# Optimization experiments

Hardware: AMD Instinct MI355X
Metric: run time of the kernel (lower is better)

## Reference

```python
import jax, jax.numpy as jnp
import numpy as np

C = 256          # channels
K = 7            # kernel_size
GC = 16          # group_channels
G = C // GC      # groups = 16
RED = C // 4     # reduction channels = 64
EPS = 1e-5


def unfold_same(x, k):
    """torch nn.Unfold(k, stride=1, padding=(k-1)//2) -> (b, c, k*k, h, w),
    channel-major patch ordering matching torch (c, kh, kw)."""
    pad = (k - 1) // 2
    xp = jnp.pad(x, ((0, 0), (0, 0), (pad, pad), (pad, pad)))
    h, w = x.shape[2], x.shape[3]
    # fixed k*k=49 slices, vectorized over all data dims
    pats = jnp.stack([xp[:, :, i:i + h, j:j + w]
                      for i in range(k) for j in range(k)], axis=2)
    return pats  # (b, c, k*k, h, w)


def setup_inputs() -> dict:
    key = jax.random.key(0)
    ks = jax.random.split(key, 8)
    b, h, w = 2, 64, 64
    feature_map = jax.random.normal(ks[0], (b, C, h, w), jnp.float32)
    guide_map = jax.random.normal(ks[1], (b, C, h, w), jnp.float32)
    # convs1: 1x1 conv (no bias, followed by BN) + BN params + ReLU
    w1 = jax.random.normal(ks[2], (RED, C), jnp.float32) * (1.0 / np.sqrt(C))
    bn_gamma = jnp.ones((RED,), jnp.float32)
    bn_beta = jnp.zeros((RED,), jnp.float32)
    bn_mean = jax.random.normal(ks[3], (RED,), jnp.float32) * 0.1
    bn_var = jax.random.uniform(ks[4], (RED,), jnp.float32, 0.5, 1.5)
    # convs2: 1x1 conv with bias, out = K^2 * G channels
    w2 = jax.random.normal(ks[5], (K * K * G, RED), jnp.float32) * (1.0 / np.sqrt(RED))
    b2 = jax.random.normal(ks[6], (K * K * G,), jnp.float32) * 0.01
    return dict(feature_map=feature_map, guide_map=guide_map,
                w1=w1, bn_gamma=bn_gamma, bn_beta=bn_beta,
                bn_mean=bn_mean, bn_var=bn_var, w2=w2, b2=b2)


def reference(feature_map, guide_map, w1, bn_gamma, bn_beta, bn_mean, bn_var, w2, b2):
    b, _, h, w = feature_map.shape
    # kernel-generation branch: 1x1 conv -> BN (inference) -> ReLU -> 1x1 conv
    t = jnp.einsum('oc,bchw->bohw', w1, guide_map)
    scale = bn_gamma / jnp.sqrt(bn_var + EPS)
    shift = bn_beta - bn_mean * scale
    t = jax.nn.relu(t * scale[None, :, None, None] + shift[None, :, None, None])
    weight = jnp.einsum('or,brhw->bohw', w2, t) + b2[None, :, None, None]
    weight = weight.reshape(b, G, K * K, h, w)
    # involution: unfold, broadcast per-pixel kernels over group channels, reduce K^2
    pats = unfold_same(feature_map, K).reshape(b, G, GC, K * K, h, w)
    out = jnp.einsum('bgkhw,bgckhw->bgchw', weight, pats).reshape(b, C, h, w)
    return out + feature_map
```

## Files before the change

kernel.cpp:

```cpp
#include <hip/hip_runtime.h>

#define CC  256
#define HW  4096
#define HH  64
#define WW  64
#define RED 64
#define K2  49
#define NG  16
#define GCH 16

typedef __attribute__((ext_vector_type(8))) short bf16x8;
typedef __attribute__((ext_vector_type(4))) float f32x4;

__device__ inline unsigned short f2bf(float f) {
    union { float f; unsigned u; } v; v.f = f;
    unsigned r = v.u + 0x7FFF + ((v.u >> 16) & 1);
    return (unsigned short)(r >> 16);
}

#define TT_ELTS   524288
#define W2BF_ROWS 832

__global__ __launch_bounds__(64) void k1_kernel(
    const float* __restrict__ guide,
    const float* __restrict__ w1,
    const float* __restrict__ gamma,
    const float* __restrict__ beta,
    const float* __restrict__ mean,
    const float* __restrict__ var,
    const float* __restrict__ w2,
    unsigned short* __restrict__ tt,
    unsigned short* __restrict__ w2bf)
{
    const int bid = blockIdx.x;
    const int tid = threadIdx.x;

    if (bid >= 512) {
        const int idx = (bid - 512) * 64 + tid;
        if (idx < (W2BF_ROWS * RED) / 8) {
            unsigned short r8[8];
            if (idx * 8 < K2 * NG * RED) {
                const float4 a = *reinterpret_cast<const float4*>(w2 + idx * 8);
                const float4 b = *reinterpret_cast<const float4*>(w2 + idx * 8 + 4);
                r8[0] = f2bf(a.x); r8[1] = f2bf(a.y); r8[2] = f2bf(a.z); r8[3] = f2bf(a.w);
                r8[4] = f2bf(b.x); r8[5] = f2bf(b.y); r8[6] = f2bf(b.z); r8[7] = f2bf(b.w);
            } else {
                #pragma unroll
                for (int i = 0; i < 8; ++i) r8[i] = 0;
            }
            *reinterpret_cast<uint4*>(w2bf + idx * 8) = *reinterpret_cast<const uint4*>(r8);
        }
        return;
    }

    const int bb = bid >> 8;
    const int y  = (bid >> 2) & 63;
    const int nt = bid & 3;
    const int lm = tid & 15;
    const int lg = tid >> 4;
    const int px = nt * 16 + lm;

    const float* gcol = guide + (size_t)bb * CC * HW + (size_t)y * WW + px;

    f32x4 acc[4] = {f32x4{0,0,0,0}, f32x4{0,0,0,0}, f32x4{0,0,0,0}, f32x4{0,0,0,0}};

    #pragma unroll
    for (int ks = 0; ks < 8; ++ks) {
        const int cbase = ks * 32 + lg * 8;
        union { unsigned short u[8]; bf16x8 v; } B;
        #pragma unroll
        for (int j = 0; j < 8; ++j)
            B.u[j] = f2bf(gcol[(size_t)(cbase + j) * HW]);
        #pragma unroll
        for (int mt = 0; mt < 4; ++mt) {
            const float* ar = w1 + (size_t)(mt * 16 + lm) * CC + cbase;
            const float4 a0 = *reinterpret_cast<const float4*>(ar);
            const float4 a1 = *reinterpret_cast<const float4*>(ar + 4);
            union { unsigned short u[8]; bf16x8 v; } A;
            A.u[0] = f2bf(a0.x); A.u[1] = f2bf(a0.y);
            A.u[2] = f2bf(a0.z); A.u[3] = f2bf(a0.w);
            A.u[4] = f2bf(a1.x); A.u[5] = f2bf(a1.y);
            A.u[6] = f2bf(a1.z); A.u[7] = f2bf(a1.w);
            acc[mt] = __builtin_amdgcn_mfma_f32_16x16x32_bf16(A.v, B.v, acc[mt], 0, 0, 0);
        }
    }

    const size_t ttrow = ((size_t)bb * HW + (size_t)y * WW + px) * RED;
    #pragma unroll
    for (int mt = 0; mt < 4; ++mt) {
        union { unsigned short u[4]; uint2 v; } R;
        #pragma unroll
        for (int rr = 0; rr < 4; ++rr) {
            const int o = mt * 16 + lg * 4 + rr;
            const float sc = gamma[o] * rsqrtf(var[o] + 1e-5f);
            const float sh = beta[o] - mean[o] * sc;
            float v = fmaf(acc[mt][rr], sc, sh);
            v = v > 0.f ? v : 0.f;
            R.u[rr] = f2bf(v);
        }
        *reinterpret_cast<uint2*>(tt + ttrow + mt * 16 + lg * 4) = R.v;
    }
}

__global__ __launch_bounds__(256, 3) void k2_inv_kernel(
    const float* __restrict__ feat,
    const unsigned short* __restrict__ tt,
    const unsigned short* __restrict__ w2bf,
    const float* __restrict__ b2,
    float* __restrict__ out)
{
    __shared__ float wg[2][K2][WW];

    const int bid = blockIdx.x;
    const int bb  = bid >> 9;
    const int y   = (bid >> 3) & 63;
    const int gp  = bid & 7;
    const int tid  = threadIdx.x;
    const int lane = tid & 63;
    const int wv   = __builtin_amdgcn_readfirstlane(tid >> 6);
    const int lm = lane & 15;
    const int lg = lane >> 4;

    {
        const int gi    = wv >> 1;
        const int g     = gp * 2 + gi;
        const int obase = g * K2;
        f32x4 acc[2][4];
        #pragma unroll
        for (int h = 0; h < 2; ++h)
            #pragma unroll
            for (int mt = 0; mt < 4; ++mt) acc[h][mt] = f32x4{0, 0, 0, 0};

        #pragma unroll
        for (int h = 0; h < 2; ++h) {
            const int nt = (wv & 1) * 2 + h;
            const size_t ttb = ((size_t)bb * HW + (size_t)y * WW + nt * 16 + lm) * RED + lg * 8;
            #pragma unroll
            for (int ks = 0; ks < 2; ++ks) {
                const bf16x8 bfr = *reinterpret_cast<const bf16x8*>(tt + ttb + ks * 32);
                #pragma unroll
                for (int mt = 0; mt < 4; ++mt) {
                    const bf16x8 afr = *reinterpret_cast<const bf16x8*>(
                        w2bf + (size_t)(obase + mt * 16 + lm) * RED + ks * 32 + lg * 8);
                    acc[h][mt] = __builtin_amdgcn_mfma_f32_16x16x32_bf16(afr, bfr, acc[h][mt], 0, 0, 0);
                }
            }
        }
        #pragma unroll
        for (int h = 0; h < 2; ++h)
            #pragma unroll
            for (int mt = 0; mt < 4; ++mt)
                #pragma unroll
                for (int rr = 0; rr < 4; ++rr) {
                    const int o2 = mt * 16 + lg * 4 + rr;
                    if (o2 < K2)
                        wg[gi][o2][(wv & 1) * 32 + h * 16 + lm] = acc[h][mt][rr] + b2[obase + o2];
                }
    }
    __syncthreads();

    const int gh = tid >> 7;
    const int cp = (tid >> 4) & 7;
    const int xq = tid & 15;
    const int x0 = xq * 4;
    const int c0 = (gp * 2 + gh) * GCH + cp * 2;
    const float* fb0 = feat + ((size_t)bb * CC + c0) * HW;
    const float* fb1 = fb0 + HW;

    const float4 rr0 = *reinterpret_cast<const float4*>(fb0 + (size_t)y * WW + x0);
    const float4 rr1 = *reinterpret_cast<const float4*>(fb1 + (size_t)y * WW + x0);
    float s00 = rr0.x, s01 = rr0.y, s02 = rr0.z, s03 = rr0.w;
    float s10 = rr1.x, s11 = rr1.y, s12 = rr1.z, s13 = rr1.w;

    #pragma unroll
    for (int i = 0; i < 7; ++i) {
        const int yy = y + i - 3;
        if (yy < 0 || yy >= HH) continue;
        const float* fr0 = fb0 + (size_t)yy * WW;
        const float* fr1 = fb1 + (size_t)yy * WW;

        float4 L0 = make_float4(0.f, 0.f, 0.f, 0.f), L1 = L0;
        float4 R0 = L0, R1 = L0;
        const float4 M0 = *reinterpret_cast<const float4*>(fr0 + x0);
        const float4 M1 = *reinterpret_cast<const float4*>(fr1 + x0);
        if (xq > 0)  { L0 = *reinterpret_cast<const float4*>(fr0 + x0 - 4);
                       L1 = *reinterpret_cast<const float4*>(fr1 + x0 - 4); }
        if (xq < 15) { R0 = *reinterpret_cast<const float4*>(fr0 + x0 + 4);
                       R1 = *reinterpret_cast<const float4*>(fr1 + x0 + 4); }
        const float b0[12] = {L0.x, L0.y, L0.z, L0.w, M0.x, M0.y, M0.z, M0.w,
                              R0.x, R0.y, R0.z, R0.w};
        const float b1[12] = {L1.x, L1.y, L1.z, L1.w, M1.x, M1.y, M1.z, M1.w,
                              R1.x, R1.y, R1.z, R1.w};

        #pragma unroll
        for (int jx = 0; jx < 7; ++jx) {
            const float4 w4 = *reinterpret_cast<const float4*>(&wg[gh][i * 7 + jx][x0]);
            s00 = fmaf(w4.x, b0[jx + 1], s00);
            s01 = fmaf(w4.y, b0[jx + 2], s01);
            s02 = fmaf(w4.z, b0[jx + 3], s02);
            s03 = fmaf(w4.w, b0[jx + 4], s03);
            s10 = fmaf(w4.x, b1[jx + 1], s10);
            s11 = fmaf(w4.y, b1[jx + 2], s11);
            s12 = fmaf(w4.z, b1[jx + 3], s12);
            s13 = fmaf(w4.w, b1[jx + 4], s13);
        }
    }

    float4 o0; o0.x = s00; o0.y = s01; o0.z = s02; o0.w = s03;
    float4 o1; o1.x = s10; o1.y = s11; o1.z = s12; o1.w = s13;
    float* ob = out + ((size_t)bb * CC + c0) * HW + (size_t)y * WW + x0;
    *reinterpret_cast<float4*>(ob)      = o0;
    *reinterpret_cast<float4*>(ob + HW) = o1;
}

__global__ __launch_bounds__(512, 1) void crossinv_fused_kernel(
    const float* __restrict__ feat, const float* __restrict__ guide,
    const float* __restrict__ w1, const float* __restrict__ gamma,
    const float* __restrict__ beta, const float* __restrict__ mean,
    const float* __restrict__ var, const float* __restrict__ w2,
    const float* __restrict__ b2, float* __restrict__ out)
{
    __shared__ float st[RED][WW];
    __shared__ float wg[K2][WW];
    const int bid  = blockIdx.x;
    const int bb   = bid >> 7;
    const int y    = (bid >> 1) & 63;
    const int gsel = bid & 1;
    const int lane = threadIdx.x & 63;
    const int wv   = __builtin_amdgcn_readfirstlane(threadIdx.x >> 6);

    const float* gptr = guide + (size_t)bb * CC * HW + (size_t)y * WW + lane;
    float acc[8];
    #pragma unroll
    for (int j = 0; j < 8; ++j) acc[j] = 0.f;
    for (int c0 = 0; c0 < CC; c0 += 4) {
        const float gv0 = gptr[(c0 + 0) * HW];
        const float gv1 = gptr[(c0 + 1) * HW];
        const float gv2 = gptr[(c0 + 2) * HW];
        const float gv3 = gptr[(c0 + 3) * HW];
        #pragma unroll
        for (int j = 0; j < 8; ++j) {
            const int o = wv + 8 * j;
            const float4 wr = *reinterpret_cast<const float4*>(w1 + o * CC + c0);
            acc[j] = fmaf(wr.x, gv0, acc[j]);
            acc[j] = fmaf(wr.y, gv1, acc[j]);
            acc[j] = fmaf(wr.z, gv2, acc[j]);
            acc[j] = fmaf(wr.w, gv3, acc[j]);
        }
    }
    #pragma unroll
    for (int j = 0; j < 8; ++j) {
        const int o = wv + 8 * j;
        const float sc = gamma[o] * rsqrtf(var[o] + 1e-5f);
        const float sh = beta[o] - mean[o] * sc;
        const float v  = fmaf(acc[j], sc, sh);
        st[o][lane] = v > 0.f ? v : 0.f;
    }
    __syncthreads();
    for (int gi = 0; gi < 8; ++gi) {
        const int gg    = gsel * 8 + gi;
        const int obase = gg * K2;
        float accw[7];
        #pragma unroll
        for (int j = 0; j < 7; ++j) {
            const int o2 = wv + 8 * j;
            accw[j] = (o2 < K2) ? b2[obase + o2] : 0.f;
        }
        for (int r0 = 0; r0 < RED; r0 += 4) {
            const float t0 = st[r0 + 0][lane];
            const float t1 = st[r0 + 1][lane];
            const float t2 = st[r0 + 2][lane];
            const float t3 = st[r0 + 3][lane];
            #pragma unroll
            for (int j = 0; j < 7; ++j) {
                const int o2 = wv + 8 * j;
                if (o2 < K2) {
                    const float4 wr = *reinterpret_cast<const float4*>(
                        w2 + (size_t)(obase + o2) * RED + r0);
                    accw[j] = fmaf(wr.x, t0, accw[j]);
                    accw[j] = fmaf(wr.y, t1, accw[j]);
                    accw[j] = fmaf(wr.z, t2, accw[j]);
                    accw[j] = fmaf(wr.w, t3, accw[j]);
                }
            }
        }
        #pragma unroll
        for (int j = 0; j < 7; ++j) {
            const int o2 = wv + 8 * j;
            if (o2 < K2) wg[o2][lane] = accw[j];
        }
        __syncthreads();
        #pragma unroll
        for (int cc2 = 0; cc2 < 2; ++cc2) {
            const int cc = wv * 2 + cc2;
            const int cch = gg * GCH + cc;
            const float* fb = feat + ((size_t)bb * CC + cch) * HW;
            float sum = fb[y * WW + lane];
            #pragma unroll
            for (int i = 0; i < 7; ++i) {
                const int yy = y + i - 3;
                if (yy < 0 || yy >= HH) continue;
                const float* frow = fb + yy * WW;
                #pragma unroll
                for (int jx = 0; jx < 7; ++jx) {
                    const int xx = lane + jx - 3;
                    const float fv = (xx >= 0 && xx < WW) ? frow[xx] : 0.f;
                    sum = fmaf(wg[i * 7 + jx][lane], fv, sum);
                }
            }
            out[((size_t)bb * CC + cch) * HW + (size_t)y * WW + lane] = sum;
        }
        __syncthreads();
    }
}

extern "C" void kernel_launch(void* const* d_in, const int* in_sizes, int n_in,
                              void* d_out, int out_size, void* d_ws, size_t ws_size,
                              hipStream_t stream) {
    const float* feat  = (const float*)d_in[0];
    const float* guide = (const float*)d_in[1];
    const float* w1    = (const float*)d_in[2];
    const float* gamma = (const float*)d_in[3];
    const float* beta  = (const float*)d_in[4];
    const float* mean  = (const float*)d_in[5];
    const float* var   = (const float*)d_in[6];
    const float* w2    = (const float*)d_in[7];
    const float* b2    = (const float*)d_in[8];
    float* out = (float*)d_out;

    const size_t need = (size_t)TT_ELTS * 2 + (size_t)W2BF_ROWS * RED * 2;
    if (ws_size >= need) {
        unsigned short* tt   = (unsigned short*)d_ws;
        unsigned short* w2bf = tt + TT_ELTS;
        hipLaunchKernelGGL(k1_kernel, dim3(512 + 104), dim3(64), 0, stream,
                           guide, w1, gamma, beta, mean, var, w2, tt, w2bf);
        hipLaunchKernelGGL(k2_inv_kernel, dim3(1024), dim3(256), 0, stream,
                           feat, tt, w2bf, b2, out);
    } else {
        hipLaunchKernelGGL(crossinv_fused_kernel, dim3(256), dim3(512), 0, stream,
                           feat, guide, w1, gamma, beta, mean, var, w2, b2, out);
    }
}
```

Measured before the change: 30.19 us.

## Tile involution over four rows per block and pack k1 into 256-thread blocks

The involution kernel now gives each block one group and four output rows instead of one row and two groups. Each loaded feature row is reused across up to four output rows, so a block reads 10 rows per channel instead of 7 per output row, and each w2bf A-fragment is reused across four column tiles in the MFMA loop. The residual add is folded into the i==3 tap. The first kernel packs four 64-lane work units into each 256-thread block, giving 154 blocks instead of 616. The trade-offs are fewer blocks (512) for the involution stage, a larger shared buffer padded to 68 columns, and more accumulator registers.

```diff
diff --git a/kernel.cpp b/kernel.cpp
--- a/kernel.cpp
+++ b/kernel.cpp
@@ -21,7 +21,7 @@
 #define TT_ELTS   524288
 #define W2BF_ROWS 832
 
-__global__ __launch_bounds__(64) void k1_kernel(
+__global__ __launch_bounds__(256) void k1_kernel(
     const float* __restrict__ guide,
     const float* __restrict__ w1,
     const float* __restrict__ gamma,
@@ -32,11 +32,11 @@
     unsigned short* __restrict__ tt,
     unsigned short* __restrict__ w2bf)
 {
-    const int bid = blockIdx.x;
-    const int tid = threadIdx.x;
-
-    if (bid >= 512) {
-        const int idx = (bid - 512) * 64 + tid;
+    const int lane = threadIdx.x & 63;
+    const int unit = blockIdx.x * 4 + __builtin_amdgcn_readfirstlane(threadIdx.x >> 6);
+
+    if (unit >= 512) {
+        const int idx = (unit - 512) * 64 + lane;
         if (idx < (W2BF_ROWS * RED) / 8) {
             unsigned short r8[8];
             if (idx * 8 < K2 * NG * RED) {
@@ -53,11 +53,11 @@
         return;
     }
 
-    const int bb = bid >> 8;
-    const int y  = (bid >> 2) & 63;
-    const int nt = bid & 3;
-    const int lm = tid & 15;
-    const int lg = tid >> 4;
+    const int bb = unit >> 8;
+    const int y  = (unit >> 2) & 63;
+    const int nt = unit & 3;
+    const int lm = lane & 15;
+    const int lg = lane >> 4;
     const int px = nt * 16 + lm;
 
     const float* gcol = guide + (size_t)bb * CC * HW + (size_t)y * WW + px;
@@ -109,108 +109,116 @@
     const float* __restrict__ b2,
     float* __restrict__ out)
 {
-    __shared__ float wg[2][K2][WW];
+    __shared__ float wg[4][K2][68];
 
     const int bid = blockIdx.x;
-    const int bb  = bid >> 9;
-    const int y   = (bid >> 3) & 63;
-    const int gp  = bid & 7;
+    const int bb  = bid >> 8;
+    const int yt  = (bid >> 4) & 15;
+    const int g   = bid & 15;
+    const int y0  = yt * 4;
     const int tid  = threadIdx.x;
     const int lane = tid & 63;
     const int wv   = __builtin_amdgcn_readfirstlane(tid >> 6);
     const int lm = lane & 15;
     const int lg = lane >> 4;
+    const int obase = g * K2;
 
     {
-        const int gi    = wv >> 1;
-        const int g     = gp * 2 + gi;
-        const int obase = g * K2;
-        f32x4 acc[2][4];
-        #pragma unroll
-        for (int h = 0; h < 2; ++h)
-            #pragma unroll
-            for (int mt = 0; mt < 4; ++mt) acc[h][mt] = f32x4{0, 0, 0, 0};
-
-        #pragma unroll
-        for (int h = 0; h < 2; ++h) {
-            const int nt = (wv & 1) * 2 + h;
-            const size_t ttb = ((size_t)bb * HW + (size_t)y * WW + nt * 16 + lm) * RED + lg * 8;
-            #pragma unroll
-            for (int ks = 0; ks < 2; ++ks) {
-                const bf16x8 bfr = *reinterpret_cast<const bf16x8*>(tt + ttb + ks * 32);
+        const int y = y0 + wv;
+        f32x4 acc[4][4];
+        #pragma unroll
+        for (int nt = 0; nt < 4; ++nt)
+            #pragma unroll
+            for (int mt = 0; mt < 4; ++mt) acc[nt][mt] = f32x4{0, 0, 0, 0};
+
+        #pragma unroll
+        for (int ks = 0; ks < 2; ++ks) {
+            bf16x8 bfr[4];
+            #pragma unroll
+            for (int nt = 0; nt < 4; ++nt)
+                bfr[nt] = *reinterpret_cast<const bf16x8*>(
+                    tt + ((size_t)bb * HW + (size_t)y * WW + nt * 16 + lm) * RED + ks * 32 + lg * 8);
+            #pragma unroll
+            for (int mt = 0; mt < 4; ++mt) {
+                const bf16x8 afr = *reinterpret_cast<const bf16x8*>(
+                    w2bf + (size_t)(obase + mt * 16 + lm) * RED + ks * 32 + lg * 8);
                 #pragma unroll
-                for (int mt = 0; mt < 4; ++mt) {
-                    const bf16x8 afr = *reinterpret_cast<const bf16x8*>(
-                        w2bf + (size_t)(obase + mt * 16 + lm) * RED + ks * 32 + lg * 8);
-                    acc[h][mt] = __builtin_amdgcn_mfma_f32_16x16x32_bf16(afr, bfr, acc[h][mt], 0, 0, 0);
-                }
-            }
-        }
-        #pragma unroll
-        for (int h = 0; h < 2; ++h)
+                for (int nt = 0; nt < 4; ++nt)
+                    acc[nt][mt] = __builtin_amdgcn_mfma_f32_16x16x32_bf16(afr, bfr[nt], acc[nt][mt], 0, 0, 0);
+            }
+        }
+        float bias[4][4];
+        #pragma unroll
+        for (int mt = 0; mt < 4; ++mt)
+            #pragma unroll
+            for (int rr = 0; rr < 4; ++rr) {
+                const int o2 = mt * 16 + lg * 4 + rr;
+                bias[mt][rr] = (o2 < K2) ? b2[obase + o2] : 0.f;
+            }
+        #pragma unroll
+        for (int nt = 0; nt < 4; ++nt)
             #pragma unroll
             for (int mt = 0; mt < 4; ++mt)
                 #pragma unroll
                 for (int rr = 0; rr < 4; ++rr) {
                     const int o2 = mt * 16 + lg * 4 + rr;
                     if (o2 < K2)
-                        wg[gi][o2][(wv & 1) * 32 + h * 16 + lm] = acc[h][mt][rr] + b2[obase + o2];
+                        wg[wv][o2][nt * 16 + lm] = acc[nt][mt][rr] + bias[mt][rr];
                 }
     }
     __syncthreads();
 
-    const int gh = tid >> 7;
-    const int cp = (tid >> 4) & 7;
+    const int cl = tid >> 4;
     const int xq = tid & 15;
     const int x0 = xq * 4;
-    const int c0 = (gp * 2 + gh) * GCH + cp * 2;
-    const float* fb0 = feat + ((size_t)bb * CC + c0) * HW;
-    const float* fb1 = fb0 + HW;
-
-    const float4 rr0 = *reinterpret_cast<const float4*>(fb0 + (size_t)y * WW + x0);
-    const float4 rr1 = *reinterpret_cast<const float4*>(fb1 + (size_t)y * WW + x0);
-    float s00 = rr0.x, s01 = rr0.y, s02 = rr0.z, s03 = rr0.w;
-    float s10 = rr1.x, s11 = rr1.y, s12 = rr1.z, s13 = rr1.w;
-
-    #pragma unroll
-    for (int i = 0; i < 7; ++i) {
-        const int yy = y + i - 3;
-        if (yy < 0 || yy >= HH) continue;
-        const float* fr0 = fb0 + (size_t)yy * WW;
-        const float* fr1 = fb1 + (size_t)yy * WW;
-
-        float4 L0 = make_float4(0.f, 0.f, 0.f, 0.f), L1 = L0;
-        float4 R0 = L0, R1 = L0;
-        const float4 M0 = *reinterpret_cast<const float4*>(fr0 + x0);
-        const float4 M1 = *reinterpret_cast<const float4*>(fr1 + x0);
-        if (xq > 0)  { L0 = *reinterpret_cast<const float4*>(fr0 + x0 - 4);
-                       L1 = *reinterpret_cast<const float4*>(fr1 + x0 - 4); }
-        if (xq < 15) { R0 = *reinterpret_cast<const float4*>(fr0 + x0 + 4);
-                       R1 = *reinterpret_cast<const float4*>(fr1 + x0 + 4); }
-        const float b0[12] = {L0.x, L0.y, L0.z, L0.w, M0.x, M0.y, M0.z, M0.w,
-                              R0.x, R0.y, R0.z, R0.w};
-        const float b1[12] = {L1.x, L1.y, L1.z, L1.w, M1.x, M1.y, M1.z, M1.w,
-                              R1.x, R1.y, R1.z, R1.w};
-
-        #pragma unroll
-        for (int jx = 0; jx < 7; ++jx) {
-            const float4 w4 = *reinterpret_cast<const float4*>(&wg[gh][i * 7 + jx][x0]);
-            s00 = fmaf(w4.x, b0[jx + 1], s00);
-            s01 = fmaf(w4.y, b0[jx + 2], s01);
-            s02 = fmaf(w4.z, b0[jx + 3], s02);
-            s03 = fmaf(w4.w, b0[jx + 4], s03);
-            s10 = fmaf(w4.x, b1[jx + 1], s10);
-            s11 = fmaf(w4.y, b1[jx + 2], s11);
-            s12 = fmaf(w4.z, b1[jx + 3], s12);
-            s13 = fmaf(w4.w, b1[jx + 4], s13);
-        }
-    }
-
-    float4 o0; o0.x = s00; o0.y = s01; o0.z = s02; o0.w = s03;
-    float4 o1; o1.x = s10; o1.y = s11; o1.z = s12; o1.w = s13;
-    float* ob = out + ((size_t)bb * CC + c0) * HW + (size_t)y * WW + x0;
-    *reinterpret_cast<float4*>(ob)      = o0;
-    *reinterpret_cast<float4*>(ob + HW) = o1;
+    const int c  = g * GCH + cl;
+    const float* fb = feat + ((size_t)bb * CC + c) * HW;
+
+    float s[4][4];
+    #pragma unroll
+    for (int ys = 0; ys < 4; ++ys)
+        #pragma unroll
+        for (int p = 0; p < 4; ++p) s[ys][p] = 0.f;
+
+    #pragma unroll
+    for (int dr = 0; dr < 10; ++dr) {
+        const int r = y0 - 3 + dr;
+        if (r < 0 || r >= HH) continue;
+        const float* fr = fb + (size_t)r * WW;
+
+        float4 L = make_float4(0.f, 0.f, 0.f, 0.f);
+        float4 Rr = L;
+        const float4 M = *reinterpret_cast<const float4*>(fr + x0);
+        if (xq > 0)  L  = *reinterpret_cast<const float4*>(fr + x0 - 4);
+        if (xq < 15) Rr = *reinterpret_cast<const float4*>(fr + x0 + 4);
+        const float buf[12] = {L.x, L.y, L.z, L.w, M.x, M.y, M.z, M.w,
+                               Rr.x, Rr.y, Rr.z, Rr.w};
+
+        #pragma unroll
+        for (int ys = 0; ys < 4; ++ys) {
+            const int i = dr - ys;
+            if (i < 0 || i >= 7) continue;
+            if (i == 3) {
+                s[ys][0] += buf[4]; s[ys][1] += buf[5];
+                s[ys][2] += buf[6]; s[ys][3] += buf[7];
+            }
+            #pragma unroll
+            for (int jx = 0; jx < 7; ++jx) {
+                const float4 w4 = *reinterpret_cast<const float4*>(&wg[ys][i * 7 + jx][x0]);
+                s[ys][0] = fmaf(w4.x, buf[jx + 1], s[ys][0]);
+                s[ys][1] = fmaf(w4.y, buf[jx + 2], s[ys][1]);
+                s[ys][2] = fmaf(w4.z, buf[jx + 3], s[ys][2]);
+                s[ys][3] = fmaf(w4.w, buf[jx + 4], s[ys][3]);
+            }
+        }
+    }
+
+    #pragma unroll
+    for (int ys = 0; ys < 4; ++ys) {
+        float4 o4; o4.x = s[ys][0]; o4.y = s[ys][1]; o4.z = s[ys][2]; o4.w = s[ys][3];
+        *reinterpret_cast<float4*>(out + ((size_t)bb * CC + c) * HW
+                                   + (size_t)(y0 + ys) * WW + x0) = o4;
+    }
 }
 
 __global__ __launch_bounds__(512, 1) void crossinv_fused_kernel(
@@ -220,8 +228,8 @@
     const float* __restrict__ var, const float* __restrict__ w2,
     const float* __restrict__ b2, float* __restrict__ out)
 {
-    __shared__ float st[RED][WW];
-    __shared__ float wg[K2][WW];
+    __shared__ float stf[RED][WW];
+    __shared__ float wgf[K2][WW];
     const int bid  = blockIdx.x;
     const int bb   = bid >> 7;
     const int y    = (bid >> 1) & 63;
@@ -254,7 +262,7 @@
         const float sc = gamma[o] * rsqrtf(var[o] + 1e-5f);
         const float sh = beta[o] - mean[o] * sc;
         const float v  = fmaf(acc[j], sc, sh);
-        st[o][lane] = v > 0.f ? v : 0.f;
+        stf[o][lane] = v > 0.f ? v : 0.f;
     }
     __syncthreads();
     for (int gi = 0; gi < 8; ++gi) {
@@ -267,10 +275,10 @@
             accw[j] = (o2 < K2) ? b2[obase + o2] : 0.f;
         }
         for (int r0 = 0; r0 < RED; r0 += 4) {
-            const float t0 = st[r0 + 0][lane];
-            const float t1 = st[r0 + 1][lane];
-            const float t2 = st[r0 + 2][lane];
-            const float t3 = st[r0 + 3][lane];
+            const float t0 = stf[r0 + 0][lane];
+            const float t1 = stf[r0 + 1][lane];
+            const float t2 = stf[r0 + 2][lane];
+            const float t3 = stf[r0 + 3][lane];
             #pragma unroll
             for (int j = 0; j < 7; ++j) {
                 const int o2 = wv + 8 * j;
@@ -287,25 +295,25 @@
         #pragma unroll
         for (int j = 0; j < 7; ++j) {
             const int o2 = wv + 8 * j;
-            if (o2 < K2) wg[o2][lane] = accw[j];
+            if (o2 < K2) wgf[o2][lane] = accw[j];
         }
         __syncthreads();
         #pragma unroll
         for (int cc2 = 0; cc2 < 2; ++cc2) {
             const int cc = wv * 2 + cc2;
             const int cch = gg * GCH + cc;
-            const float* fb = feat + ((size_t)bb * CC + cch) * HW;
-            float sum = fb[y * WW + lane];
+            const float* fbp = feat + ((size_t)bb * CC + cch) * HW;
+            float sum = fbp[y * WW + lane];
             #pragma unroll
             for (int i = 0; i < 7; ++i) {
                 const int yy = y + i - 3;
                 if (yy < 0 || yy >= HH) continue;
-                const float* frow = fb + yy * WW;
+                const float* frow = fbp + yy * WW;
                 #pragma unroll
                 for (int jx = 0; jx < 7; ++jx) {
                     const int xx = lane + jx - 3;
                     const float fv = (xx >= 0 && xx < WW) ? frow[xx] : 0.f;
-                    sum = fmaf(wg[i * 7 + jx][lane], fv, sum);
+                    sum = fmaf(wgf[i * 7 + jx][lane], fv, sum);
                 }
             }
             out[((size_t)bb * CC + cch) * HW + (size_t)y * WW + lane] = sum;
@@ -332,9 +340,9 @@
     if (ws_size >= need) {
         unsigned short* tt   = (unsigned short*)d_ws;
         unsigned short* w2bf = tt + TT_ELTS;
-        hipLaunchKernelGGL(k1_kernel, dim3(512 + 104), dim3(64), 0, stream,
+        hipLaunchKernelGGL(k1_kernel, dim3(154), dim3(256), 0, stream,
                            guide, w1, gamma, beta, mean, var, w2, tt, w2bf);
-        hipLaunchKernelGGL(k2_inv_kernel, dim3(1024), dim3(256), 0, stream,
+        hipLaunchKernelGGL(k2_inv_kernel, dim3(512), dim3(256), 0, stream,
                            feat, tt, w2bf, b2, out);
     } else {
         hipLaunchKernelGGL(crossinv_fused_kernel, dim3(256), dim3(512), 0, stream,
```

Result: slower. 67.00 us (+121.9%).
